# Performance work log

Hardware: AMD Instinct MI355X
Metric: run time of the kernel (lower is better)

Reference implementation:

```python
import jax, jax.numpy as jnp
import numpy as np


def _chamfer_pair(x, y):
    # x: [N,3], y: [M,3] -> per-point squared NN distances (dist1 [N], dist2 [M])
    # d_ij = |x_i|^2 + |y_j|^2 - 2 x_i . y_j
    d = (jnp.sum(x * x, axis=1)[:, None]
         + jnp.sum(y * y, axis=1)[None, :]
         - 2.0 * (x @ y.T))  # [N, M]
    return jnp.min(d, axis=1), jnp.min(d, axis=0)


def setup_inputs() -> dict:
    key = jax.random.key(0)
    k1, k2 = jax.random.split(key)
    B, N, M = 4, 8192, 8192
    xyz1 = jax.random.normal(k1, (B, N, 3), dtype=jnp.float32)
    xyz2 = jax.random.normal(k2, (B, M, 3), dtype=jnp.float32)
    return {"xyz1": xyz1, "xyz2": xyz2}


def reference(xyz1, xyz2):
    # lax.map over batch keeps peak memory to one [N,M] matrix at a time,
    # mirroring the tiled custom-kernel structure of ChamferFunction.
    dist1, dist2 = jax.lax.map(lambda ab: _chamfer_pair(ab[0], ab[1]), (xyz1, xyz2))
    return jnp.mean(dist1) + jnp.mean(dist2)
```

## Files before the change

### kernel.cpp

```cpp
#include <hip/hip_runtime.h>


#define BATCH 4
#define NPTS 8192
#define TPB 256
#define NFRAG 2
#define COLS_PER_WAVE 64
#define COLS_PER_BLOCK 256
#define XBLKS (NPTS / COLS_PER_BLOCK)
#define YSEGS 8
#define YSEG (NPTS / YSEGS)
#define CHUNK 512
#define NCHUNK (YSEG / CHUNK)
#define JT (CHUNK / 32)

typedef __attribute__((ext_vector_type(8))) short bf16x8;
typedef __attribute__((ext_vector_type(16))) float f32x16;
union FragU { int4 i4; bf16x8 v; };

__device__ inline unsigned short bf16_rne(float f) {
    unsigned int u = __float_as_uint(f);
    return (unsigned short)((u + 0x7FFFu + ((u >> 16) & 1u)) >> 16);
}
__device__ inline float bf16_f32(unsigned short h) {
    return __uint_as_float(((unsigned int)h) << 16);
}
__device__ inline unsigned int pack2(unsigned int lo, unsigned int hi) {
    return (lo & 0xFFFFu) | (hi << 16);
}

__global__ __launch_bounds__(256) void prepack_kernel(
    const float* __restrict__ xyz1, const float* __restrict__ xyz2,
    int4* __restrict__ rowpack, int4* __restrict__ colpack,
    unsigned int* __restrict__ keys, unsigned int* __restrict__ counter)
{
    const int id  = blockIdx.x * 256 + threadIdx.x;
    const int arr = id >> 15;
    const int rem = id & 32767;
    const float* p = (arr ? xyz2 : xyz1) + (size_t)rem * 3;
    const float x0 = p[0], x1 = p[1], x2 = p[2];

    keys[id] = 0xFFFFFFFFu;
    if (id == 0) *counter = 0;

    const unsigned short h0 = bf16_rne(x0), h1 = bf16_rne(x1), h2 = bf16_rne(x2);
    const unsigned short l0 = bf16_rne(x0 - bf16_f32(h0));
    const unsigned short l1 = bf16_rne(x1 - bf16_f32(h1));
    const unsigned short l2 = bf16_rne(x2 - bf16_f32(h2));
    const float s = x0 * x0 + x1 * x1 + x2 * x2;
    const unsigned short sh = bf16_rne(s);
    const unsigned short sl = bf16_rne(s - bf16_f32(sh));
    const unsigned short one = 0x3F80;

    int4 rlo, rhi;
    rlo.x = pack2(h0, h1); rlo.y = pack2(h2, h0);
    rlo.z = pack2(h1, h2); rlo.w = pack2(l0, l1);
    rhi.x = pack2(l2, one); rhi.y = pack2(one, sh);
    rhi.z = pack2(sl, 0u);  rhi.w = 0;
    rowpack[2 * id]     = rlo;
    rowpack[2 * id + 1] = rhi;

    const float g0 = -2.0f * x0, g1 = -2.0f * x1, g2 = -2.0f * x2;
    const unsigned short gh0 = bf16_rne(g0), gh1 = bf16_rne(g1), gh2 = bf16_rne(g2);
    const unsigned short gl0 = bf16_rne(g0 - bf16_f32(gh0));
    const unsigned short gl1 = bf16_rne(g1 - bf16_f32(gh1));
    const unsigned short gl2 = bf16_rne(g2 - bf16_f32(gh2));
    int4 clo, chi;
    clo.x = pack2(gh0, gh1); clo.y = pack2(gh2, gl0);
    clo.z = pack2(gl1, gl2); clo.w = pack2(gh0, gh1);
    chi.x = pack2(gh2, sh);  chi.y = pack2(sl, one);
    chi.z = pack2(one, 0u);  chi.w = 0;
    colpack[2 * id]     = clo;
    colpack[2 * id + 1] = chi;
}

__device__ inline float red16(float cb, const f32x16& d) {
    const float m0 = fminf(fminf(d[0],  d[1]),  d[2]);
    const float m1 = fminf(fminf(d[3],  d[4]),  d[5]);
    const float m2 = fminf(fminf(d[6],  d[7]),  d[8]);
    const float m3 = fminf(fminf(d[9],  d[10]), d[11]);
    const float m4 = fminf(fminf(d[12], d[13]), d[14]);
    const float u0 = fminf(fminf(m0, m1), m2);
    const float u1 = fminf(fminf(m3, m4), d[15]);
    return fminf(fminf(cb, u0), u1);
}

__global__ __launch_bounds__(TPB, 8) void chamfer_main(
    const int4* __restrict__ rowpack,
    const int4* __restrict__ colpack,
    unsigned int* __restrict__ keys)
{
    const int blk  = blockIdx.x;
    const int seg  = blk & (YSEGS - 1);
    const int xblk = (blk >> 3) & (XBLKS - 1);
    const int b    = (blk >> 8) & (BATCH - 1);
    const int dir  = blk >> 10;
    const int arrB = dir;
    const int arrA = dir ^ 1;

    const int t = threadIdx.x, lane = t & 63, wave = t >> 6;
    const int half = lane >> 5, l31 = lane & 31;

    __shared__ int4 sb0[CHUNK];
    __shared__ int4 sb1[CHUNK];

    const int xbase = xblk * COLS_PER_BLOCK + wave * COLS_PER_WAVE;
    const size_t cb_idx = ((size_t)(arrB * BATCH + b) * NPTS + xbase) * 2;
    FragU bf0, bf1;
    bf0.i4 = colpack[cb_idx + (size_t)(0 * 32 + l31) * 2 + half];
    bf1.i4 = colpack[cb_idx + (size_t)(1 * 32 + l31) * 2 + half];

    float cb0 = __builtin_inff();
    float cb1 = __builtin_inff();
    const f32x16 zero = {0.0f, 0.0f, 0.0f, 0.0f, 0.0f, 0.0f, 0.0f, 0.0f,
                         0.0f, 0.0f, 0.0f, 0.0f, 0.0f, 0.0f, 0.0f, 0.0f};

    const size_t rbase = ((size_t)(arrA * BATCH + b) * NPTS + (size_t)seg * YSEG) * 2;

    for (int c = 0; c < NCHUNK; ++c) {
        __syncthreads();
        {
            const int4* src = rowpack + rbase + (size_t)c * CHUNK * 2 + (size_t)t * 4;
            const int4 a0 = src[0], a1 = src[1], a2 = src[2], a3 = src[3];
            sb0[2 * t]     = a0;  sb1[2 * t]     = a1;
            sb0[2 * t + 1] = a2;  sb1[2 * t + 1] = a3;
        }
        __syncthreads();

        const int4* asrc = half ? sb1 : sb0;
#pragma unroll 4
        for (int jt = 0; jt < JT; ++jt) {
            FragU af; af.i4 = asrc[jt * 32 + l31];
            f32x16 d0 = __builtin_amdgcn_mfma_f32_32x32x16_bf16(af.v, bf0.v, zero, 0, 0, 0);
            f32x16 d1 = __builtin_amdgcn_mfma_f32_32x32x16_bf16(af.v, bf1.v, zero, 0, 0, 0);
            cb0 = red16(cb0, d0);
            cb1 = red16(cb1, d1);
        }
    }

    unsigned int* ok = keys + ((size_t)dir * BATCH + b) * NPTS + xbase;
    {
        const float v0 = fminf(cb0, __shfl_xor(cb0, 32, 64));
        const float v1 = fminf(cb1, __shfl_xor(cb1, 32, 64));
        if (half == 0) {
            unsigned int u = __float_as_uint(v0);
            atomicMin(&ok[l31], u ^ ((u >> 31) ? 0xFFFFFFFFu : 0x80000000u));
            u = __float_as_uint(v1);
            atomicMin(&ok[32 + l31], u ^ ((u >> 31) ? 0xFFFFFFFFu : 0x80000000u));
        }
    }
}

__device__ inline float key_decode(unsigned int key) {
    const unsigned int u = (key & 0x80000000u) ? (key ^ 0x80000000u) : ~key;
    return __uint_as_float(u);
}

__global__ __launch_bounds__(1024) void reduce_kernel(
    const unsigned int* __restrict__ keys,
    unsigned long long* __restrict__ partials,
    unsigned int* __restrict__ counter,
    float* __restrict__ out)
{
    const uint4* v1 = (const uint4*)keys;
    const uint4* v2 = (const uint4*)(keys + BATCH * NPTS);
    const int idx = blockIdx.x * 1024 + threadIdx.x;
    const uint4 a = v1[idx];
    const uint4 c = v2[idx];
    double s1 = (double)key_decode(a.x) + (double)key_decode(a.y)
              + (double)key_decode(a.z) + (double)key_decode(a.w);
    double s2 = (double)key_decode(c.x) + (double)key_decode(c.y)
              + (double)key_decode(c.z) + (double)key_decode(c.w);
    for (int off = 32; off > 0; off >>= 1) {
        s1 += __shfl_down(s1, off, 64);
        s2 += __shfl_down(s2, off, 64);
    }
    __shared__ double l1[16], l2[16];
    const int wave = threadIdx.x >> 6;
    if ((threadIdx.x & 63) == 0) { l1[wave] = s1; l2[wave] = s2; }
    __syncthreads();
    if (threadIdx.x == 0) {
        double t1 = 0.0, t2 = 0.0;
        for (int w = 0; w < 16; ++w) { t1 += l1[w]; t2 += l2[w]; }
        atomicExch(&partials[2 * blockIdx.x],     (unsigned long long)__double_as_longlong(t1));
        atomicExch(&partials[2 * blockIdx.x + 1], (unsigned long long)__double_as_longlong(t2));
        __threadfence();
        const unsigned int old = atomicAdd(counter, 1u);
        if (old == 7u) {
            double g1 = 0.0, g2 = 0.0;
            for (int w = 0; w < 8; ++w) {
                g1 += __longlong_as_double((long long)atomicAdd(&partials[2 * w],     0ull));
                g2 += __longlong_as_double((long long)atomicAdd(&partials[2 * w + 1], 0ull));
            }
            const double n = (double)(BATCH * NPTS);
            out[0] = (float)(g1 / n + g2 / n);
        }
    }
}

extern "C" void kernel_launch(void* const* d_in, const int* in_sizes, int n_in,
                              void* d_out, int out_size, void* d_ws, size_t ws_size,
                              hipStream_t stream) {
    const float* xyz1 = (const float*)d_in[0];
    const float* xyz2 = (const float*)d_in[1];
    float* out = (float*)d_out;

    int4* rowpack = (int4*)d_ws;
    int4* colpack = rowpack + 2 * 65536;
    unsigned int* keys = (unsigned int*)(colpack + 2 * 65536);
    unsigned long long* partials = (unsigned long long*)(keys + 2 * BATCH * NPTS);
    unsigned int* counter = (unsigned int*)(partials + 16);

    prepack_kernel<<<256, 256, 0, stream>>>(xyz1, xyz2, rowpack, colpack, keys, counter);

    chamfer_main<<<2 * BATCH * XBLKS * YSEGS, TPB, 0, stream>>>(rowpack, colpack, keys);

    reduce_kernel<<<8, 1024, 0, stream>>>(keys, partials, counter, out);
}
```

Before: 34.14 us.

## Fuse prepack, chamfer and reduction into one kernel with in-block min

Replaces the three-kernel pipeline (prepack, MFMA main, reduce) with a single 1024-thread-per-block kernel. Each block packs its columns and row chunks to split bf16 fragments on the fly and covers the full opposite point set across four wave groups. The groups combine their per-column minima in shared memory, which removes the global atomicMin keys and the separate reduce pass; the final sum goes through a last-block-done counter. The cost is redundant row packing in every block and a smaller grid of 256 blocks, plus a memset to reset the counter.

Measured after the change: 36.59 us. +7.2%, slower.

```diff
diff --git a/kernel.cpp b/kernel.cpp
--- a/kernel.cpp
+++ b/kernel.cpp
@@ -3,16 +3,13 @@
 
 #define BATCH 4
 #define NPTS 8192
-#define TPB 256
-#define NFRAG 2
-#define COLS_PER_WAVE 64
-#define COLS_PER_BLOCK 256
-#define XBLKS (NPTS / COLS_PER_BLOCK)
-#define YSEGS 8
-#define YSEG (NPTS / YSEGS)
+#define TPB 1024
+#define GRID 256
+#define XBLKS 32
+#define YQ 2048
 #define CHUNK 512
-#define NCHUNK (YSEG / CHUNK)
-#define JT (CHUNK / 32)
+#define NCHUNK 4
+#define JT 16
 
 typedef __attribute__((ext_vector_type(8))) short bf16x8;
 typedef __attribute__((ext_vector_type(16))) float f32x16;
@@ -27,51 +24,6 @@
 }
 __device__ inline unsigned int pack2(unsigned int lo, unsigned int hi) {
     return (lo & 0xFFFFu) | (hi << 16);
-}
-
-__global__ __launch_bounds__(256) void prepack_kernel(
-    const float* __restrict__ xyz1, const float* __restrict__ xyz2,
-    int4* __restrict__ rowpack, int4* __restrict__ colpack,
-    unsigned int* __restrict__ keys, unsigned int* __restrict__ counter)
-{
-    const int id  = blockIdx.x * 256 + threadIdx.x;
-    const int arr = id >> 15;
-    const int rem = id & 32767;
-    const float* p = (arr ? xyz2 : xyz1) + (size_t)rem * 3;
-    const float x0 = p[0], x1 = p[1], x2 = p[2];
-
-    keys[id] = 0xFFFFFFFFu;
-    if (id == 0) *counter = 0;
-
-    const unsigned short h0 = bf16_rne(x0), h1 = bf16_rne(x1), h2 = bf16_rne(x2);
-    const unsigned short l0 = bf16_rne(x0 - bf16_f32(h0));
-    const unsigned short l1 = bf16_rne(x1 - bf16_f32(h1));
-    const unsigned short l2 = bf16_rne(x2 - bf16_f32(h2));
-    const float s = x0 * x0 + x1 * x1 + x2 * x2;
-    const unsigned short sh = bf16_rne(s);
-    const unsigned short sl = bf16_rne(s - bf16_f32(sh));
-    const unsigned short one = 0x3F80;
-
-    int4 rlo, rhi;
-    rlo.x = pack2(h0, h1); rlo.y = pack2(h2, h0);
-    rlo.z = pack2(h1, h2); rlo.w = pack2(l0, l1);
-    rhi.x = pack2(l2, one); rhi.y = pack2(one, sh);
-    rhi.z = pack2(sl, 0u);  rhi.w = 0;
-    rowpack[2 * id]     = rlo;
-    rowpack[2 * id + 1] = rhi;
-
-    const float g0 = -2.0f * x0, g1 = -2.0f * x1, g2 = -2.0f * x2;
-    const unsigned short gh0 = bf16_rne(g0), gh1 = bf16_rne(g1), gh2 = bf16_rne(g2);
-    const unsigned short gl0 = bf16_rne(g0 - bf16_f32(gh0));
-    const unsigned short gl1 = bf16_rne(g1 - bf16_f32(gh1));
-    const unsigned short gl2 = bf16_rne(g2 - bf16_f32(gh2));
-    int4 clo, chi;
-    clo.x = pack2(gh0, gh1); clo.y = pack2(gh2, gl0);
-    clo.z = pack2(gl1, gl2); clo.w = pack2(gh0, gh1);
-    chi.x = pack2(gh2, sh);  chi.y = pack2(sl, one);
-    chi.z = pack2(one, 0u);  chi.w = 0;
-    colpack[2 * id]     = clo;
-    colpack[2 * id + 1] = chi;
 }
 
 __device__ inline float red16(float cb, const f32x16& d) {
@@ -85,49 +37,102 @@
     return fminf(fminf(cb, u0), u1);
 }
 
-__global__ __launch_bounds__(TPB, 8) void chamfer_main(
-    const int4* __restrict__ rowpack,
-    const int4* __restrict__ colpack,
-    unsigned int* __restrict__ keys)
+__device__ inline void pack_row(float x0, float x1, float x2,
+                                int4& rlo, int4& rhi) {
+    const unsigned short h0 = bf16_rne(x0), h1 = bf16_rne(x1), h2 = bf16_rne(x2);
+    const unsigned short l0 = bf16_rne(x0 - bf16_f32(h0));
+    const unsigned short l1 = bf16_rne(x1 - bf16_f32(h1));
+    const unsigned short l2 = bf16_rne(x2 - bf16_f32(h2));
+    const float s = x0 * x0 + x1 * x1 + x2 * x2;
+    const unsigned short sh = bf16_rne(s);
+    const unsigned short sl = bf16_rne(s - bf16_f32(sh));
+    const unsigned short one = 0x3F80;
+    rlo.x = pack2(h0, h1); rlo.y = pack2(h2, h0);
+    rlo.z = pack2(h1, h2); rlo.w = pack2(l0, l1);
+    rhi.x = pack2(l2, one); rhi.y = pack2(one, sh);
+    rhi.z = pack2(sl, 0u);  rhi.w = 0;
+}
+
+__device__ inline void pack_col(float x0, float x1, float x2,
+                                int4& clo, int4& chi) {
+    const float s = x0 * x0 + x1 * x1 + x2 * x2;
+    const unsigned short sh = bf16_rne(s);
+    const unsigned short sl = bf16_rne(s - bf16_f32(sh));
+    const float g0 = -2.0f * x0, g1 = -2.0f * x1, g2 = -2.0f * x2;
+    const unsigned short gh0 = bf16_rne(g0), gh1 = bf16_rne(g1), gh2 = bf16_rne(g2);
+    const unsigned short gl0 = bf16_rne(g0 - bf16_f32(gh0));
+    const unsigned short gl1 = bf16_rne(g1 - bf16_f32(gh1));
+    const unsigned short gl2 = bf16_rne(g2 - bf16_f32(gh2));
+    const unsigned short one = 0x3F80;
+    clo.x = pack2(gh0, gh1); clo.y = pack2(gh2, gl0);
+    clo.z = pack2(gl1, gl2); clo.w = pack2(gh0, gh1);
+    chi.x = pack2(gh2, sh);  chi.y = pack2(sl, one);
+    chi.z = pack2(one, 0u);  chi.w = 0;
+}
+
+__global__ __launch_bounds__(TPB) void chamfer_one(
+    const float* __restrict__ xyz1,
+    const float* __restrict__ xyz2,
+    unsigned long long* __restrict__ partials,
+    unsigned int* __restrict__ counter,
+    float* __restrict__ out)
 {
     const int blk  = blockIdx.x;
-    const int seg  = blk & (YSEGS - 1);
-    const int xblk = (blk >> 3) & (XBLKS - 1);
-    const int b    = (blk >> 8) & (BATCH - 1);
-    const int dir  = blk >> 10;
-    const int arrB = dir;
-    const int arrA = dir ^ 1;
-
-    const int t = threadIdx.x, lane = t & 63, wave = t >> 6;
+    const int xblk = blk & (XBLKS - 1);
+    const int b    = (blk >> 5) & (BATCH - 1);
+    const int dir  = blk >> 7;
+
+    const float* colsrc = dir ? xyz2 : xyz1;
+    const float* rowsrc = dir ? xyz1 : xyz2;
+
+    const int t    = threadIdx.x;
+    const int lane = t & 63;
+    const int w    = t >> 6;
+    const int g    = w >> 2;
+    const int wl   = w & 3;
     const int half = lane >> 5, l31 = lane & 31;
 
-    __shared__ int4 sb0[CHUNK];
-    __shared__ int4 sb1[CHUNK];
-
-    const int xbase = xblk * COLS_PER_BLOCK + wave * COLS_PER_WAVE;
-    const size_t cb_idx = ((size_t)(arrB * BATCH + b) * NPTS + xbase) * 2;
+    __shared__ int4  sb0[4][CHUNK];
+    __shared__ int4  sb1[4][CHUNK];
+    __shared__ float part[4][256];
+    __shared__ double red[16];
+    __shared__ unsigned int lastflag;
+
     FragU bf0, bf1;
-    bf0.i4 = colpack[cb_idx + (size_t)(0 * 32 + l31) * 2 + half];
-    bf1.i4 = colpack[cb_idx + (size_t)(1 * 32 + l31) * 2 + half];
+    {
+        const int cbase = xblk * 256 + wl * 64 + l31;
+        const float* p0 = colsrc + ((size_t)b * NPTS + cbase) * 3;
+        const float* p1 = colsrc + ((size_t)b * NPTS + cbase + 32) * 3;
+        int4 clo, chi;
+        pack_col(p0[0], p0[1], p0[2], clo, chi);
+        bf0.i4 = half ? chi : clo;
+        pack_col(p1[0], p1[1], p1[2], clo, chi);
+        bf1.i4 = half ? chi : clo;
+    }
 
     float cb0 = __builtin_inff();
     float cb1 = __builtin_inff();
     const f32x16 zero = {0.0f, 0.0f, 0.0f, 0.0f, 0.0f, 0.0f, 0.0f, 0.0f,
                          0.0f, 0.0f, 0.0f, 0.0f, 0.0f, 0.0f, 0.0f, 0.0f};
 
-    const size_t rbase = ((size_t)(arrA * BATCH + b) * NPTS + (size_t)seg * YSEG) * 2;
+    const int tid256 = t & 255;
+    const int sg     = t >> 8;
+    const float* rbase = rowsrc + ((size_t)b * NPTS + (size_t)sg * YQ) * 3;
 
     for (int c = 0; c < NCHUNK; ++c) {
         __syncthreads();
         {
-            const int4* src = rowpack + rbase + (size_t)c * CHUNK * 2 + (size_t)t * 4;
-            const int4 a0 = src[0], a1 = src[1], a2 = src[2], a3 = src[3];
-            sb0[2 * t]     = a0;  sb1[2 * t]     = a1;
-            sb0[2 * t + 1] = a2;  sb1[2 * t + 1] = a3;
+            const int p = tid256 * 2;
+            const float* s0 = rbase + ((size_t)c * CHUNK + p) * 3;
+            int4 rlo, rhi;
+            pack_row(s0[0], s0[1], s0[2], rlo, rhi);
+            sb0[sg][p]     = rlo;  sb1[sg][p]     = rhi;
+            pack_row(s0[3], s0[4], s0[5], rlo, rhi);
+            sb0[sg][p + 1] = rlo;  sb1[sg][p + 1] = rhi;
         }
         __syncthreads();
 
-        const int4* asrc = half ? sb1 : sb0;
+        const int4* asrc = half ? sb1[g] : sb0[g];
 #pragma unroll 4
         for (int jt = 0; jt < JT; ++jt) {
             FragU af; af.i4 = asrc[jt * 32 + l31];
@@ -138,62 +143,46 @@
         }
     }
 
-    unsigned int* ok = keys + ((size_t)dir * BATCH + b) * NPTS + xbase;
     {
         const float v0 = fminf(cb0, __shfl_xor(cb0, 32, 64));
         const float v1 = fminf(cb1, __shfl_xor(cb1, 32, 64));
         if (half == 0) {
-            unsigned int u = __float_as_uint(v0);
-            atomicMin(&ok[l31], u ^ ((u >> 31) ? 0xFFFFFFFFu : 0x80000000u));
-            u = __float_as_uint(v1);
-            atomicMin(&ok[32 + l31], u ^ ((u >> 31) ? 0xFFFFFFFFu : 0x80000000u));
-        }
-    }
-}
-
-__device__ inline float key_decode(unsigned int key) {
-    const unsigned int u = (key & 0x80000000u) ? (key ^ 0x80000000u) : ~key;
-    return __uint_as_float(u);
-}
-
-__global__ __launch_bounds__(1024) void reduce_kernel(
-    const unsigned int* __restrict__ keys,
-    unsigned long long* __restrict__ partials,
-    unsigned int* __restrict__ counter,
-    float* __restrict__ out)
-{
-    const uint4* v1 = (const uint4*)keys;
-    const uint4* v2 = (const uint4*)(keys + BATCH * NPTS);
-    const int idx = blockIdx.x * 1024 + threadIdx.x;
-    const uint4 a = v1[idx];
-    const uint4 c = v2[idx];
-    double s1 = (double)key_decode(a.x) + (double)key_decode(a.y)
-              + (double)key_decode(a.z) + (double)key_decode(a.w);
-    double s2 = (double)key_decode(c.x) + (double)key_decode(c.y)
-              + (double)key_decode(c.z) + (double)key_decode(c.w);
-    for (int off = 32; off > 0; off >>= 1) {
-        s1 += __shfl_down(s1, off, 64);
-        s2 += __shfl_down(s2, off, 64);
-    }
-    __shared__ double l1[16], l2[16];
-    const int wave = threadIdx.x >> 6;
-    if ((threadIdx.x & 63) == 0) { l1[wave] = s1; l2[wave] = s2; }
+            part[g][wl * 64 + l31]      = v0;
+            part[g][wl * 64 + 32 + l31] = v1;
+        }
+    }
     __syncthreads();
-    if (threadIdx.x == 0) {
-        double t1 = 0.0, t2 = 0.0;
-        for (int w = 0; w < 16; ++w) { t1 += l1[w]; t2 += l2[w]; }
-        atomicExch(&partials[2 * blockIdx.x],     (unsigned long long)__double_as_longlong(t1));
-        atomicExch(&partials[2 * blockIdx.x + 1], (unsigned long long)__double_as_longlong(t2));
+
+    double s = 0.0;
+    if (t < 256) {
+        const float m = fminf(fminf(part[0][t], part[1][t]),
+                              fminf(part[2][t], part[3][t]));
+        s = (double)m;
+    }
+    for (int off = 32; off > 0; off >>= 1) s += __shfl_down(s, off, 64);
+    if ((t & 63) == 0) red[w] = s;
+    __syncthreads();
+    if (t == 0) {
+        double bs = 0.0;
+        for (int i = 0; i < 16; ++i) bs += red[i];
+        atomicExch(&partials[blk], (unsigned long long)__double_as_longlong(bs));
         __threadfence();
-        const unsigned int old = atomicAdd(counter, 1u);
-        if (old == 7u) {
-            double g1 = 0.0, g2 = 0.0;
-            for (int w = 0; w < 8; ++w) {
-                g1 += __longlong_as_double((long long)atomicAdd(&partials[2 * w],     0ull));
-                g2 += __longlong_as_double((long long)atomicAdd(&partials[2 * w + 1], 0ull));
+        lastflag = (atomicAdd(counter, 1u) == GRID - 1) ? 1u : 0u;
+    }
+    __syncthreads();
+
+    if (lastflag) {
+        if (w == 0) {
+            double fs = 0.0;
+#pragma unroll
+            for (int i = 0; i < 4; ++i) {
+                const unsigned long long pv =
+                    atomicAdd(&partials[lane * 4 + i], 0ull);
+                fs += __longlong_as_double((long long)pv);
             }
-            const double n = (double)(BATCH * NPTS);
-            out[0] = (float)(g1 / n + g2 / n);
+            for (int off = 32; off > 0; off >>= 1) fs += __shfl_down(fs, off, 64);
+            if (lane == 0)
+                out[0] = (float)(fs / (double)(BATCH * NPTS));
         }
     }
 }
@@ -205,15 +194,10 @@
     const float* xyz2 = (const float*)d_in[1];
     float* out = (float*)d_out;
 
-    int4* rowpack = (int4*)d_ws;
-    int4* colpack = rowpack + 2 * 65536;
-    unsigned int* keys = (unsigned int*)(colpack + 2 * 65536);
-    unsigned long long* partials = (unsigned long long*)(keys + 2 * BATCH * NPTS);
-    unsigned int* counter = (unsigned int*)(partials + 16);
-
-    prepack_kernel<<<256, 256, 0, stream>>>(xyz1, xyz2, rowpack, colpack, keys, counter);
-
-    chamfer_main<<<2 * BATCH * XBLKS * YSEGS, TPB, 0, stream>>>(rowpack, colpack, keys);
-
-    reduce_kernel<<<8, 1024, 0, stream>>>(keys, partials, counter, out);
-}
+    unsigned long long* partials = (unsigned long long*)d_ws;
+    unsigned int* counter = (unsigned int*)(partials + GRID);
+
+    hipMemsetAsync(counter, 0, sizeof(unsigned int), stream);
+
+    chamfer_one<<<GRID, TPB, 0, stream>>>(xyz1, xyz2, partials, counter, out);
+}
```
